# Kernel tuning notes

Measured on AMD Instinct MI355X. Metric: run time of the kernel, lower is better.

The kernel has to match this reference:

```python
import jax, jax.numpy as jnp
import numpy as np

B = 16384      # batch
T = 14         # number of embedding tables
L = 100000     # rows per table (table has L+1 rows due to the +1 offset)
E = 16         # em_size
H = 50         # user click history length


def setup_inputs() -> dict:
    key = jax.random.key(0)
    ks = jax.random.split(key, 10)
    sparse_features = jax.random.randint(ks[0], (B, T), 0, L, dtype=jnp.int32)
    dense_features = jax.random.normal(ks[1], (B, 1), dtype=jnp.float32)
    user_click_history = jax.random.randint(ks[2], (B, H), 0, L, dtype=jnp.int32)
    # stacked EmbeddingBag weights: [T, L+1, E]
    W = jax.random.normal(ks[3], (T, L + 1, E), dtype=jnp.float32) * 0.01
    fc1_w = jax.random.normal(ks[4], (200, 241), dtype=jnp.float32) / np.sqrt(241).astype(np.float32)
    fc1_b = jnp.zeros((200,), jnp.float32)
    fc2_w = jax.random.normal(ks[5], (80, 200), dtype=jnp.float32) / np.sqrt(200).astype(np.float32)
    fc2_b = jnp.zeros((80,), jnp.float32)
    fc3_w = jax.random.normal(ks[6], (2, 80), dtype=jnp.float32) / np.sqrt(80).astype(np.float32)
    fc3_b = jnp.zeros((2,), jnp.float32)
    return dict(sparse_features=sparse_features, dense_features=dense_features,
                user_click_history=user_click_history, W=W,
                fc1_w=fc1_w, fc1_b=fc1_b, fc2_w=fc2_w, fc2_b=fc2_b,
                fc3_w=fc3_w, fc3_b=fc3_b)


def reference(sparse_features, dense_features, user_click_history, W,
              fc1_w, fc1_b, fc2_w, fc2_b, fc3_w, fc3_b):
    # Per-table single-index EmbeddingBag(sum) == plain lookup. Batched gather
    # across all T tables at once: [B, T, E]
    embs = W[jnp.arange(T)[None, :], sparse_features + 1]
    embs = embs.reshape(embs.shape[0], T * E)  # [B, T*E]
    # tables[0].weight row 0 is zeroed before the history lookup (padding row).
    W0 = W[0].at[0].set(0.0)
    hist = W0[user_click_history + 1].sum(axis=1)  # [B, E] EmbeddingBag sum
    x = jnp.concatenate([embs, hist, dense_features], axis=1)  # [B, 241]
    x = jax.nn.relu(x @ fc1_w.T + fc1_b)
    x = jax.nn.relu(x @ fc2_w.T + fc2_b)
    return x @ fc3_w.T + fc3_b  # [B, 2]
```

## Files before the change

### kernel.cpp

```cpp
#include <hip/hip_runtime.h>


using u16 = unsigned short;
typedef __attribute__((ext_vector_type(8))) short short8v;
typedef __attribute__((ext_vector_type(4))) short short4v;
typedef __attribute__((ext_vector_type(4))) float floatx4;

constexpr int W1_ELEMS = 13 * 8 * 64 * 8;
constexpr int W2_ELEMS = 5 * 7 * 64 * 8;
constexpr int W0_ROWS = 100001;
constexpr int W0_ELEMS = W0_ROWS * 16;

__device__ __forceinline__ u16 f2bf(float f) {
  unsigned u = __float_as_uint(f);
  unsigned r = (u + 0x7fffu + ((u >> 16) & 1u)) >> 16;
  return (u16)r;
}
__device__ __forceinline__ float bf2f(u16 h) {
  return __uint_as_float(((unsigned)h) << 16);
}

__global__ void precompute(const float* __restrict__ w1, const float* __restrict__ w2,
                           const float* __restrict__ W,
                           u16* __restrict__ w1h, u16* __restrict__ w2h,
                           u16* __restrict__ w0b) {
  int b = blockIdx.x;
  if (b < 35) {
    int tid = b * 256 + threadIdx.x;
    if (tid < 13 * 8 * 64) {
      int l = tid & 63;
      int g = tid >> 6;
      int kt = g & 7, nt = g >> 3;
      int n = nt * 16 + (l & 15);
      int kb = kt * 32 + (l >> 4) * 8;
      short8v h8;
#pragma unroll
      for (int e = 0; e < 8; ++e) {
        int k = kb + e;
        float v = (n < 200 && k < 241) ? w1[n * 241 + k] : 0.f;
        h8[e] = (short)f2bf(v);
      }
      *(short8v*)&w1h[tid * 8] = h8;
    } else if (tid < 13 * 8 * 64 + 5 * 7 * 64) {
      int t2 = tid - 13 * 8 * 64;
      int l = t2 & 63;
      int g = t2 >> 6;
      int kt = g % 7, nt = g / 7;
      int n = nt * 16 + (l & 15);
      int kb = kt * 32 + (l >> 4) * 8;
      short8v h8;
#pragma unroll
      for (int e = 0; e < 8; ++e) {
        int k = kb + e;
        float v = (k < 200) ? w2[n * 200 + k] : 0.f;
        h8[e] = (short)f2bf(v);
      }
      *(short8v*)&w2h[t2 * 8] = h8;
    }
  } else {
    int t = (b - 35) * 256 + threadIdx.x;
    int base = t * 8;
    if (base < W0_ELEMS) {
      floatx4 f0 = *(const floatx4*)(W + base);
      floatx4 f1 = *(const floatx4*)(W + base + 4);
      short8v o;
      o[0] = (short)f2bf(f0[0]);
      o[1] = (short)f2bf(f0[1]);
      o[2] = (short)f2bf(f0[2]);
      o[3] = (short)f2bf(f0[3]);
      o[4] = (short)f2bf(f1[0]);
      o[5] = (short)f2bf(f1[1]);
      o[6] = (short)f2bf(f1[2]);
      o[7] = (short)f2bf(f1[3]);
      *(short8v*)(w0b + base) = o;
    }
  }
}

__global__ __launch_bounds__(256, 4) void fused_kernel(
    const int* __restrict__ sf, const float* __restrict__ dense,
    const int* __restrict__ hist, const float* __restrict__ W,
    const u16* __restrict__ w0b,
    const u16* __restrict__ w1h, const u16* __restrict__ w2h,
    const float* __restrict__ b1, const float* __restrict__ b2,
    const float* __restrict__ w3, const float* __restrict__ b3,
    float* __restrict__ out) {
  __shared__ u16 A1h[8 * 64 * 8];
  __shared__ u16 A1l7[64 * 8];
  __shared__ u16 A2h[7 * 64 * 8], A2l[7 * 64 * 8];
  __shared__ float o2[16 * 84];

  const int tid = threadIdx.x;
  const int l = tid & 63;
  const int wv = tid >> 6;
  const int row0 = blockIdx.x * 16;
  short8v z8 = {0, 0, 0, 0, 0, 0, 0, 0};

  const int ntbase = (wv == 0) ? 0 : 4 + 3 * (wv - 1);
  const int ntcnt = (wv == 0) ? 4 : 3;

  short8v bhr[2][4];
#pragma unroll
  for (int kk = 0; kk < 2; ++kk)
#pragma unroll
    for (int i = 0; i < 4; ++i)
      bhr[kk][i] = (i < ntcnt) ? *(const short8v*)&w1h[(((ntbase + i) * 8 + kk) * 64 + l) * 8]
                               : z8;

#pragma unroll
  for (int it = 0; it < 4; ++it) {
    int g = tid + it * 256;
    if (g < 896) {
      int q = g & 3, rt = g >> 2;
      int r = rt & 15, t = rt >> 4;
      int idx = sf[(row0 + r) * 14 + t] + 1;
      const floatx4 v4 = *(const floatx4*)(W + ((size_t)t * 100001 + (size_t)idx) * 16 + q * 4);
      int k0 = t * 16 + q * 4;
      int kt = k0 >> 5, kg = (k0 >> 3) & 3, e0 = k0 & 7;
      short4v h4;
#pragma unroll
      for (int d = 0; d < 4; ++d) h4[d] = (short)f2bf(v4[d]);
      *(short4v*)&A1h[(kt * 64 + kg * 16 + r) * 8 + e0] = h4;
    }
  }

  {
    int r = tid >> 4, rem = tid & 15, q = rem & 1, s = rem >> 1;
    const int* hp = hist + (row0 + r) * 50;
    const u16* Wq = w0b + q * 8;
    float a[8] = {0.f, 0.f, 0.f, 0.f, 0.f, 0.f, 0.f, 0.f};
#pragma unroll
    for (int hh = 0; hh < 6; ++hh) {
      int idx = hp[s + hh * 8] + 1;
      short8v v = *(const short8v*)(Wq + (size_t)idx * 16);
#pragma unroll
      for (int d = 0; d < 8; ++d) a[d] += bf2f((u16)v[d]);
    }
    if (s < 2) {
      int idx = hp[48 + s] + 1;
      short8v v = *(const short8v*)(Wq + (size_t)idx * 16);
#pragma unroll
      for (int d = 0; d < 8; ++d) a[d] += bf2f((u16)v[d]);
    }
#pragma unroll
    for (int d = 0; d < 8; ++d) {
      a[d] += __shfl_xor(a[d], 2);
      a[d] += __shfl_xor(a[d], 4);
      a[d] += __shfl_xor(a[d], 8);
    }
    if (s == 0) {
      short8v h8, l8;
#pragma unroll
      for (int d = 0; d < 8; ++d) {
        u16 hi = f2bf(a[d]);
        h8[d] = (short)hi;
        l8[d] = (short)f2bf(a[d] - bf2f(hi));
      }
      *(short8v*)&A1h[(7 * 64 + q * 16 + r) * 8] = h8;
      *(short8v*)&A1l7[(q * 16 + r) * 8] = l8;
      if (q == 0) {
        float dv = dense[row0 + r];
        u16 dh = f2bf(dv), dl = f2bf(dv - bf2f(dh));
        short8v dh8 = z8, dl8 = z8;
        dh8[0] = (short)dh;
        dl8[0] = (short)dl;
        *(short8v*)&A1h[(7 * 64 + 32 + r) * 8] = dh8;
        *(short8v*)&A1l7[(32 + r) * 8] = dl8;
        *(short8v*)&A1h[(7 * 64 + 48 + r) * 8] = z8;
        *(short8v*)&A1l7[(48 + r) * 8] = z8;
      }
    }
  }
  __syncthreads();

  floatx4 acc[4];
#pragma unroll
  for (int i = 0; i < 4; ++i) acc[i] = (floatx4){0.f, 0.f, 0.f, 0.f};

#pragma unroll
  for (int kt = 0; kt < 8; ++kt) {
    short8v ah = *(const short8v*)&A1h[(kt * 64 + l) * 8];
    short8v al7;
    if (kt == 7) al7 = *(const short8v*)&A1l7[l * 8];
#pragma unroll
    for (int i = 0; i < 4; ++i) {
      if (i < ntcnt) {
        short8v cb = bhr[kt & 1][i];
        if (kt < 6) bhr[kt & 1][i] = *(const short8v*)&w1h[(((ntbase + i) * 8 + kt + 2) * 64 + l) * 8];
        acc[i] = __builtin_amdgcn_mfma_f32_16x16x32_bf16(ah, cb, acc[i], 0, 0, 0);
        if (kt == 7) acc[i] = __builtin_amdgcn_mfma_f32_16x16x32_bf16(al7, cb, acc[i], 0, 0, 0);
      }
    }
  }

  const int ntA = wv;
  short8v bra[2], brb[2];
  bra[0] = *(const short8v*)&w2h[((ntA * 7 + 0) * 64 + l) * 8];
  bra[1] = *(const short8v*)&w2h[((ntA * 7 + 1) * 64 + l) * 8];
  if (wv == 0) {
    brb[0] = *(const short8v*)&w2h[((4 * 7 + 0) * 64 + l) * 8];
    brb[1] = *(const short8v*)&w2h[((4 * 7 + 1) * 64 + l) * 8];
  } else {
    brb[0] = z8;
    brb[1] = z8;
  }

#pragma unroll
  for (int i = 0; i < 4; ++i) {
    if (i < ntcnt) {
      int n = (ntbase + i) * 16 + (l & 15);
      float bias = (n < 200) ? b1[n] : 0.f;
#pragma unroll
      for (int g = 0; g < 4; ++g) {
        float v = (n < 200) ? fmaxf(acc[i][g] + bias, 0.f) : 0.f;
        int m = (l >> 4) * 4 + g;
        u16 hi = f2bf(v), lo = f2bf(v - bf2f(hi));
        int kt2 = n >> 5, kg2 = (n >> 3) & 3, e = n & 7;
        int pos = (kt2 * 64 + kg2 * 16 + m) * 8 + e;
        A2h[pos] = hi;
        A2l[pos] = lo;
      }
    }
  }
  if (wv == 1 && l < 32) {
    *(short8v*)&A2h[(6 * 64 + 32 + l) * 8] = z8;
    *(short8v*)&A2l[(6 * 64 + 32 + l) * 8] = z8;
  }
  __syncthreads();

  floatx4 acca = (floatx4){0.f, 0.f, 0.f, 0.f};
  floatx4 accb = (floatx4){0.f, 0.f, 0.f, 0.f};
#pragma unroll
  for (int kt = 0; kt < 7; ++kt) {
    short8v ah = *(const short8v*)&A2h[(kt * 64 + l) * 8];
    short8v al = *(const short8v*)&A2l[(kt * 64 + l) * 8];
    short8v ca = bra[kt & 1];
    if (kt < 5) bra[kt & 1] = *(const short8v*)&w2h[((ntA * 7 + kt + 2) * 64 + l) * 8];
    acca = __builtin_amdgcn_mfma_f32_16x16x32_bf16(ah, ca, acca, 0, 0, 0);
    acca = __builtin_amdgcn_mfma_f32_16x16x32_bf16(al, ca, acca, 0, 0, 0);
    if (wv == 0) {
      short8v cb = brb[kt & 1];
      if (kt < 5) brb[kt & 1] = *(const short8v*)&w2h[((4 * 7 + kt + 2) * 64 + l) * 8];
      accb = __builtin_amdgcn_mfma_f32_16x16x32_bf16(ah, cb, accb, 0, 0, 0);
      accb = __builtin_amdgcn_mfma_f32_16x16x32_bf16(al, cb, accb, 0, 0, 0);
    }
  }

  {
    int n = ntA * 16 + (l & 15);
    float bias = b2[n];
#pragma unroll
    for (int g = 0; g < 4; ++g) {
      int r = (l >> 4) * 4 + g;
      o2[r * 84 + n] = fmaxf(acca[g] + bias, 0.f);
    }
    if (wv == 0) {
      int n2 = 64 + (l & 15);
      float bias2 = b2[n2];
#pragma unroll
      for (int g = 0; g < 4; ++g) {
        int r = (l >> 4) * 4 + g;
        o2[r * 84 + n2] = fmaxf(accb[g] + bias2, 0.f);
      }
    }
  }
  __syncthreads();

  if (tid < 32) {
    int r = tid >> 1, o = tid & 1;
    float a = b3[o];
    const float* orow = &o2[r * 84];
    const float* wrow = &w3[o * 80];
#pragma unroll
    for (int j = 0; j < 80; j += 4) {
      floatx4 xv = *(const floatx4*)&orow[j];
      floatx4 wv4 = *(const floatx4*)&wrow[j];
      a += xv[0] * wv4[0] + xv[1] * wv4[1] + xv[2] * wv4[2] + xv[3] * wv4[3];
    }
    out[(row0 + r) * 2 + o] = a;
  }
}

extern "C" void kernel_launch(void* const* d_in, const int* in_sizes, int n_in,
                              void* d_out, int out_size, void* d_ws, size_t ws_size,
                              hipStream_t stream) {
  const int* sf = (const int*)d_in[0];
  const float* dense = (const float*)d_in[1];
  const int* hist = (const int*)d_in[2];
  const float* W = (const float*)d_in[3];
  const float* w1 = (const float*)d_in[4];
  const float* b1 = (const float*)d_in[5];
  const float* w2 = (const float*)d_in[6];
  const float* b2 = (const float*)d_in[7];
  const float* w3 = (const float*)d_in[8];
  const float* b3 = (const float*)d_in[9];
  float* out = (float*)d_out;

  u16* w1h = (u16*)d_ws;
  u16* w2h = w1h + W1_ELEMS;
  u16* w0b = w2h + W2_ELEMS;

  int conv_blocks = (W0_ELEMS / 8 + 255) / 256;
  precompute<<<dim3(35 + conv_blocks), dim3(256), 0, stream>>>(w1, w2, W, w1h, w2h, w0b);
  fused_kernel<<<dim3(1024), dim3(256), 0, stream>>>(sf, dense, hist, W, w0b, w1h, w2h,
                                                     b1, b2, w3, b3, out);
}
```

Before: 30.28 us.

## Move sparse embedding gather into prep kernel with MFMA-ready layout

The per-table embedding gather and bf16 conversion move out of the fused MLP kernel into the prep kernel, which writes them to a workspace buffer already laid out as MFMA A-fragments per 16-row tile. The MLP kernel then loads these fragments straight into registers, with no LDS staging for the first seven K tiles. The aim is to run the latency-bound random gathers alongside the weight conversion and shrink the MLP kernel's LDS use. In exchange it adds an extra global write and read of about 7 MB and extends the prep kernel.

```diff
diff --git a/kernel.cpp b/kernel.cpp
--- a/kernel.cpp
+++ b/kernel.cpp
@@ -10,6 +10,7 @@
 constexpr int W2_ELEMS = 5 * 7 * 64 * 8;
 constexpr int W0_ROWS = 100001;
 constexpr int W0_ELEMS = W0_ROWS * 16;
+constexpr int EF_ELEMS = 1024 * 7 * 64 * 8;
 
 __device__ __forceinline__ u16 f2bf(float f) {
   unsigned u = __float_as_uint(f);
@@ -20,10 +21,10 @@
   return __uint_as_float(((unsigned)h) << 16);
 }
 
-__global__ void precompute(const float* __restrict__ w1, const float* __restrict__ w2,
-                           const float* __restrict__ W,
-                           u16* __restrict__ w1h, u16* __restrict__ w2h,
-                           u16* __restrict__ w0b) {
+__global__ void prep_kernel(const float* __restrict__ w1, const float* __restrict__ w2,
+                            const float* __restrict__ W, const int* __restrict__ sf,
+                            u16* __restrict__ w1h, u16* __restrict__ w2h,
+                            u16* __restrict__ w0b, u16* __restrict__ ef) {
   int b = blockIdx.x;
   if (b < 35) {
     int tid = b * 256 + threadIdx.x;
@@ -57,7 +58,7 @@
       }
       *(short8v*)&w2h[t2 * 8] = h8;
     }
-  } else {
+  } else if (b < 35 + 782) {
     int t = (b - 35) * 256 + threadIdx.x;
     int base = t * 8;
     if (base < W0_ELEMS) {
@@ -74,30 +75,48 @@
       o[7] = (short)f2bf(f1[3]);
       *(short8v*)(w0b + base) = o;
     }
-  }
-}
-
-__global__ __launch_bounds__(256, 4) void fused_kernel(
-    const int* __restrict__ sf, const float* __restrict__ dense,
-    const int* __restrict__ hist, const float* __restrict__ W,
-    const u16* __restrict__ w0b,
+  } else {
+    int g = (b - 817) * 256 + threadIdx.x;
+    int t = g >> 16;
+    int bb = (g >> 2) & 16383;
+    int q = g & 3;
+    int idx = sf[bb * 14 + t] + 1;
+    floatx4 v4 = *(const floatx4*)(W + ((size_t)t * 100001 + (size_t)idx) * 16 + q * 4);
+    short4v h4;
+#pragma unroll
+    for (int d = 0; d < 4; ++d) h4[d] = (short)f2bf(v4[d]);
+    int k0 = t * 16 + q * 4;
+    int kt = k0 >> 5, kg = (k0 >> 3) & 3, e0 = k0 & 7;
+    int tile = bb >> 4, r = bb & 15;
+    *(short4v*)&ef[((tile * 7 + kt) * 64 + kg * 16 + r) * 8 + e0] = h4;
+  }
+}
+
+__global__ __launch_bounds__(256, 4) void mlp_kernel(
+    const float* __restrict__ dense, const int* __restrict__ hist,
+    const u16* __restrict__ w0b, const u16* __restrict__ ef,
     const u16* __restrict__ w1h, const u16* __restrict__ w2h,
     const float* __restrict__ b1, const float* __restrict__ b2,
     const float* __restrict__ w3, const float* __restrict__ b3,
     float* __restrict__ out) {
-  __shared__ u16 A1h[8 * 64 * 8];
-  __shared__ u16 A1l7[64 * 8];
+  __shared__ u16 A1h7[64 * 8], A1l7[64 * 8];
   __shared__ u16 A2h[7 * 64 * 8], A2l[7 * 64 * 8];
   __shared__ float o2[16 * 84];
 
   const int tid = threadIdx.x;
   const int l = tid & 63;
   const int wv = tid >> 6;
-  const int row0 = blockIdx.x * 16;
+  const int tile = blockIdx.x;
+  const int row0 = tile * 16;
   short8v z8 = {0, 0, 0, 0, 0, 0, 0, 0};
 
   const int ntbase = (wv == 0) ? 0 : 4 + 3 * (wv - 1);
   const int ntcnt = (wv == 0) ? 4 : 3;
+
+  short8v ga[7];
+#pragma unroll
+  for (int kt = 0; kt < 7; ++kt)
+    ga[kt] = *(const short8v*)&ef[((tile * 7 + kt) * 64 + l) * 8];
 
   short8v bhr[2][4];
 #pragma unroll
@@ -106,23 +125,6 @@
     for (int i = 0; i < 4; ++i)
       bhr[kk][i] = (i < ntcnt) ? *(const short8v*)&w1h[(((ntbase + i) * 8 + kk) * 64 + l) * 8]
                                : z8;
-
-#pragma unroll
-  for (int it = 0; it < 4; ++it) {
-    int g = tid + it * 256;
-    if (g < 896) {
-      int q = g & 3, rt = g >> 2;
-      int r = rt & 15, t = rt >> 4;
-      int idx = sf[(row0 + r) * 14 + t] + 1;
-      const floatx4 v4 = *(const floatx4*)(W + ((size_t)t * 100001 + (size_t)idx) * 16 + q * 4);
-      int k0 = t * 16 + q * 4;
-      int kt = k0 >> 5, kg = (k0 >> 3) & 3, e0 = k0 & 7;
-      short4v h4;
-#pragma unroll
-      for (int d = 0; d < 4; ++d) h4[d] = (short)f2bf(v4[d]);
-      *(short4v*)&A1h[(kt * 64 + kg * 16 + r) * 8 + e0] = h4;
-    }
-  }
 
   {
     int r = tid >> 4, rem = tid & 15, q = rem & 1, s = rem >> 1;
@@ -156,7 +158,7 @@
         h8[d] = (short)hi;
         l8[d] = (short)f2bf(a[d] - bf2f(hi));
       }
-      *(short8v*)&A1h[(7 * 64 + q * 16 + r) * 8] = h8;
+      *(short8v*)&A1h7[(q * 16 + r) * 8] = h8;
       *(short8v*)&A1l7[(q * 16 + r) * 8] = l8;
       if (q == 0) {
         float dv = dense[row0 + r];
@@ -164,9 +166,9 @@
         short8v dh8 = z8, dl8 = z8;
         dh8[0] = (short)dh;
         dl8[0] = (short)dl;
-        *(short8v*)&A1h[(7 * 64 + 32 + r) * 8] = dh8;
+        *(short8v*)&A1h7[(32 + r) * 8] = dh8;
         *(short8v*)&A1l7[(32 + r) * 8] = dl8;
-        *(short8v*)&A1h[(7 * 64 + 48 + r) * 8] = z8;
+        *(short8v*)&A1h7[(48 + r) * 8] = z8;
         *(short8v*)&A1l7[(48 + r) * 8] = z8;
       }
     }
@@ -179,7 +181,7 @@
 
 #pragma unroll
   for (int kt = 0; kt < 8; ++kt) {
-    short8v ah = *(const short8v*)&A1h[(kt * 64 + l) * 8];
+    short8v ah = (kt < 7) ? ga[kt] : *(const short8v*)&A1h7[l * 8];
     short8v al7;
     if (kt == 7) al7 = *(const short8v*)&A1l7[l * 8];
 #pragma unroll
@@ -299,9 +301,9 @@
   u16* w1h = (u16*)d_ws;
   u16* w2h = w1h + W1_ELEMS;
   u16* w0b = w2h + W2_ELEMS;
-
-  int conv_blocks = (W0_ELEMS / 8 + 255) / 256;
-  precompute<<<dim3(35 + conv_blocks), dim3(256), 0, stream>>>(w1, w2, W, w1h, w2h, w0b);
-  fused_kernel<<<dim3(1024), dim3(256), 0, stream>>>(sf, dense, hist, W, w0b, w1h, w2h,
-                                                     b1, b2, w3, b3, out);
-}
+  u16* ef = w0b + W0_ELEMS;
+
+  prep_kernel<<<dim3(35 + 782 + 3584), dim3(256), 0, stream>>>(w1, w2, W, sf, w1h, w2h, w0b, ef);
+  mlp_kernel<<<dim3(1024), dim3(256), 0, stream>>>(dense, hist, w0b, ef, w1h, w2h,
+                                                   b1, b2, w3, b3, out);
+}
```

Measured after the change: 30.49 us. Within noise of the previous version (+0.7%).

## Process two row tiles per block, prefetching second tile's gathers during first compute

Applied to the files above, without the earlier changes.

The fused kernel is split into gather-issue, gather-finish and compute helpers. Each block now handles 32 rows as two 16-row tiles. The embedding and history loads for the second tile are issued into registers before the first tile's MLP compute, and the A1 staging buffers in shared memory are double-buffered. The aim is to hide gather latency behind MFMA work, at the cost of halving the grid to 512 blocks, lowering launch-bounds occupancy and using more registers.

```diff
diff --git a/kernel.cpp b/kernel.cpp
--- a/kernel.cpp
+++ b/kernel.cpp
@@ -8,8 +8,7 @@
 
 constexpr int W1_ELEMS = 13 * 8 * 64 * 8;
 constexpr int W2_ELEMS = 5 * 7 * 64 * 8;
-constexpr int W0_ROWS = 100001;
-constexpr int W0_ELEMS = W0_ROWS * 16;
+constexpr int W0_ELEMS = 100001 * 16;
 
 __device__ __forceinline__ u16 f2bf(float f) {
   unsigned u = __float_as_uint(f);
@@ -77,25 +76,104 @@
   }
 }
 
-__global__ __launch_bounds__(256, 4) void fused_kernel(
-    const int* __restrict__ sf, const float* __restrict__ dense,
-    const int* __restrict__ hist, const float* __restrict__ W,
-    const u16* __restrict__ w0b,
-    const u16* __restrict__ w1h, const u16* __restrict__ w2h,
+struct GatherRegs {
+  floatx4 ev[4];
+  short8v hv[7];
+  float dv;
+};
+
+__device__ __forceinline__ void gather_issue(const int* __restrict__ sf,
+                                             const int* __restrict__ hist,
+                                             const float* __restrict__ dense,
+                                             const float* __restrict__ W,
+                                             const u16* __restrict__ w0b,
+                                             int row0, int tid, GatherRegs& gr) {
+#pragma unroll
+  for (int it = 0; it < 4; ++it) {
+    int g = tid + it * 256;
+    if (g < 896) {
+      int q = g & 3, rt = g >> 2, r = rt & 15, t = rt >> 4;
+      int idx = sf[(row0 + r) * 14 + t] + 1;
+      gr.ev[it] = *(const floatx4*)(W + ((size_t)t * 100001 + (size_t)idx) * 16 + q * 4);
+    }
+  }
+  int r = tid >> 4, rem = tid & 15, q = rem & 1, s = rem >> 1;
+  const int* hp = hist + (row0 + r) * 50;
+  const u16* Wq = w0b + q * 8;
+#pragma unroll
+  for (int hh = 0; hh < 6; ++hh) {
+    int idx = hp[s + hh * 8] + 1;
+    gr.hv[hh] = *(const short8v*)(Wq + (size_t)idx * 16);
+  }
+  if (s < 2) {
+    int idx = hp[48 + s] + 1;
+    gr.hv[6] = *(const short8v*)(Wq + (size_t)idx * 16);
+  }
+  gr.dv = dense[row0 + r];
+}
+
+__device__ __forceinline__ void gather_finish(int tid, const GatherRegs& gr,
+                                              u16* A1hb, u16* A1l7b) {
+  short8v z8 = {0, 0, 0, 0, 0, 0, 0, 0};
+#pragma unroll
+  for (int it = 0; it < 4; ++it) {
+    int g = tid + it * 256;
+    if (g < 896) {
+      int q = g & 3, rt = g >> 2, r = rt & 15, t = rt >> 4;
+      int k0 = t * 16 + q * 4, kt = k0 >> 5, kg = (k0 >> 3) & 3, e0 = k0 & 7;
+      short4v h4;
+#pragma unroll
+      for (int d = 0; d < 4; ++d) h4[d] = (short)f2bf(gr.ev[it][d]);
+      *(short4v*)&A1hb[(kt * 64 + kg * 16 + r) * 8 + e0] = h4;
+    }
+  }
+  int r = tid >> 4, rem = tid & 15, q = rem & 1, s = rem >> 1;
+  float a[8] = {0.f, 0.f, 0.f, 0.f, 0.f, 0.f, 0.f, 0.f};
+#pragma unroll
+  for (int hh = 0; hh < 6; ++hh)
+#pragma unroll
+    for (int d = 0; d < 8; ++d) a[d] += bf2f((u16)gr.hv[hh][d]);
+  if (s < 2)
+#pragma unroll
+    for (int d = 0; d < 8; ++d) a[d] += bf2f((u16)gr.hv[6][d]);
+#pragma unroll
+  for (int d = 0; d < 8; ++d) {
+    a[d] += __shfl_xor(a[d], 2);
+    a[d] += __shfl_xor(a[d], 4);
+    a[d] += __shfl_xor(a[d], 8);
+  }
+  if (s == 0) {
+    short8v h8, l8;
+#pragma unroll
+    for (int d = 0; d < 8; ++d) {
+      u16 hi = f2bf(a[d]);
+      h8[d] = (short)hi;
+      l8[d] = (short)f2bf(a[d] - bf2f(hi));
+    }
+    *(short8v*)&A1hb[(7 * 64 + q * 16 + r) * 8] = h8;
+    *(short8v*)&A1l7b[(q * 16 + r) * 8] = l8;
+    if (q == 0) {
+      u16 dh = f2bf(gr.dv), dl = f2bf(gr.dv - bf2f(dh));
+      short8v dh8 = z8, dl8 = z8;
+      dh8[0] = (short)dh;
+      dl8[0] = (short)dl;
+      *(short8v*)&A1hb[(7 * 64 + 32 + r) * 8] = dh8;
+      *(short8v*)&A1l7b[(32 + r) * 8] = dl8;
+      *(short8v*)&A1hb[(7 * 64 + 48 + r) * 8] = z8;
+      *(short8v*)&A1l7b[(48 + r) * 8] = z8;
+    }
+  }
+}
+
+__device__ __forceinline__ void compute_tile(
+    const u16* A1hb, const u16* A1l7b, u16* A2h, u16* A2l, float* o2,
+    int row0, int tid, const u16* __restrict__ w1h, const u16* __restrict__ w2h,
     const float* __restrict__ b1, const float* __restrict__ b2,
     const float* __restrict__ w3, const float* __restrict__ b3,
     float* __restrict__ out) {
-  __shared__ u16 A1h[8 * 64 * 8];
-  __shared__ u16 A1l7[64 * 8];
-  __shared__ u16 A2h[7 * 64 * 8], A2l[7 * 64 * 8];
-  __shared__ float o2[16 * 84];
-
-  const int tid = threadIdx.x;
   const int l = tid & 63;
   const int wv = tid >> 6;
-  const int row0 = blockIdx.x * 16;
   short8v z8 = {0, 0, 0, 0, 0, 0, 0, 0};
-
   const int ntbase = (wv == 0) ? 0 : 4 + 3 * (wv - 1);
   const int ntcnt = (wv == 0) ? 4 : 3;
 
@@ -107,81 +185,15 @@
       bhr[kk][i] = (i < ntcnt) ? *(const short8v*)&w1h[(((ntbase + i) * 8 + kk) * 64 + l) * 8]
                                : z8;
 
-#pragma unroll
-  for (int it = 0; it < 4; ++it) {
-    int g = tid + it * 256;
-    if (g < 896) {
-      int q = g & 3, rt = g >> 2;
-      int r = rt & 15, t = rt >> 4;
-      int idx = sf[(row0 + r) * 14 + t] + 1;
-      const floatx4 v4 = *(const floatx4*)(W + ((size_t)t * 100001 + (size_t)idx) * 16 + q * 4);
-      int k0 = t * 16 + q * 4;
-      int kt = k0 >> 5, kg = (k0 >> 3) & 3, e0 = k0 & 7;
-      short4v h4;
-#pragma unroll
-      for (int d = 0; d < 4; ++d) h4[d] = (short)f2bf(v4[d]);
-      *(short4v*)&A1h[(kt * 64 + kg * 16 + r) * 8 + e0] = h4;
-    }
-  }
-
-  {
-    int r = tid >> 4, rem = tid & 15, q = rem & 1, s = rem >> 1;
-    const int* hp = hist + (row0 + r) * 50;
-    const u16* Wq = w0b + q * 8;
-    float a[8] = {0.f, 0.f, 0.f, 0.f, 0.f, 0.f, 0.f, 0.f};
-#pragma unroll
-    for (int hh = 0; hh < 6; ++hh) {
-      int idx = hp[s + hh * 8] + 1;
-      short8v v = *(const short8v*)(Wq + (size_t)idx * 16);
-#pragma unroll
-      for (int d = 0; d < 8; ++d) a[d] += bf2f((u16)v[d]);
-    }
-    if (s < 2) {
-      int idx = hp[48 + s] + 1;
-      short8v v = *(const short8v*)(Wq + (size_t)idx * 16);
-#pragma unroll
-      for (int d = 0; d < 8; ++d) a[d] += bf2f((u16)v[d]);
-    }
-#pragma unroll
-    for (int d = 0; d < 8; ++d) {
-      a[d] += __shfl_xor(a[d], 2);
-      a[d] += __shfl_xor(a[d], 4);
-      a[d] += __shfl_xor(a[d], 8);
-    }
-    if (s == 0) {
-      short8v h8, l8;
-#pragma unroll
-      for (int d = 0; d < 8; ++d) {
-        u16 hi = f2bf(a[d]);
-        h8[d] = (short)hi;
-        l8[d] = (short)f2bf(a[d] - bf2f(hi));
-      }
-      *(short8v*)&A1h[(7 * 64 + q * 16 + r) * 8] = h8;
-      *(short8v*)&A1l7[(q * 16 + r) * 8] = l8;
-      if (q == 0) {
-        float dv = dense[row0 + r];
-        u16 dh = f2bf(dv), dl = f2bf(dv - bf2f(dh));
-        short8v dh8 = z8, dl8 = z8;
-        dh8[0] = (short)dh;
-        dl8[0] = (short)dl;
-        *(short8v*)&A1h[(7 * 64 + 32 + r) * 8] = dh8;
-        *(short8v*)&A1l7[(32 + r) * 8] = dl8;
-        *(short8v*)&A1h[(7 * 64 + 48 + r) * 8] = z8;
-        *(short8v*)&A1l7[(48 + r) * 8] = z8;
-      }
-    }
-  }
-  __syncthreads();
-
   floatx4 acc[4];
 #pragma unroll
   for (int i = 0; i < 4; ++i) acc[i] = (floatx4){0.f, 0.f, 0.f, 0.f};
 
 #pragma unroll
   for (int kt = 0; kt < 8; ++kt) {
-    short8v ah = *(const short8v*)&A1h[(kt * 64 + l) * 8];
+    short8v ah = *(const short8v*)&A1hb[(kt * 64 + l) * 8];
     short8v al7;
-    if (kt == 7) al7 = *(const short8v*)&A1l7[l * 8];
+    if (kt == 7) al7 = *(const short8v*)&A1l7b[l * 8];
 #pragma unroll
     for (int i = 0; i < 4; ++i) {
       if (i < ntcnt) {
@@ -279,6 +291,39 @@
     }
     out[(row0 + r) * 2 + o] = a;
   }
+}
+
+__global__ __launch_bounds__(256, 2) void mlp_kernel(
+    const int* __restrict__ sf, const float* __restrict__ dense,
+    const int* __restrict__ hist, const float* __restrict__ W,
+    const u16* __restrict__ w0b, const u16* __restrict__ w1h,
+    const u16* __restrict__ w2h, const float* __restrict__ b1,
+    const float* __restrict__ b2, const float* __restrict__ w3,
+    const float* __restrict__ b3, float* __restrict__ out) {
+  __shared__ u16 A1h[2][8 * 64 * 8];
+  __shared__ u16 A1l7[2][64 * 8];
+  __shared__ u16 A2h[7 * 64 * 8], A2l[7 * 64 * 8];
+  __shared__ float o2[16 * 84];
+
+  const int tid = threadIdx.x;
+  const int row0 = blockIdx.x * 32;
+
+  GatherRegs gr0;
+  gather_issue(sf, hist, dense, W, w0b, row0, tid, gr0);
+  gather_finish(tid, gr0, A1h[0], A1l7[0]);
+  __syncthreads();
+
+  GatherRegs gr1;
+  gather_issue(sf, hist, dense, W, w0b, row0 + 16, tid, gr1);
+
+  compute_tile(A1h[0], A1l7[0], A2h, A2l, o2, row0, tid,
+               w1h, w2h, b1, b2, w3, b3, out);
+
+  gather_finish(tid, gr1, A1h[1], A1l7[1]);
+  __syncthreads();
+
+  compute_tile(A1h[1], A1l7[1], A2h, A2l, o2, row0 + 16, tid,
+               w1h, w2h, b1, b2, w3, b3, out);
 }
 
 extern "C" void kernel_launch(void* const* d_in, const int* in_sizes, int n_in,
@@ -302,6 +347,6 @@
 
   int conv_blocks = (W0_ELEMS / 8 + 255) / 256;
   precompute<<<dim3(35 + conv_blocks), dim3(256), 0, stream>>>(w1, w2, W, w1h, w2h, w0b);
-  fused_kernel<<<dim3(1024), dim3(256), 0, stream>>>(sf, dense, hist, W, w0b, w1h, w2h,
-                                                     b1, b2, w3, b3, out);
-}
+  mlp_kernel<<<dim3(512), dim3(256), 0, stream>>>(sf, dense, hist, W, w0b, w1h, w2h,
+                                                  b1, b2, w3, b3, out);
+}
```

Measured after the change: 36.27 us. 19.8% more time.
